# Performance work log

Measured on AMD Instinct MI355X. Metric: run time of the kernel, lower is better.

Reference implementation:

```python
import jax, jax.numpy as jnp
import numpy as np

N = 64   # SSM state size
H = 256  # channels
B = 8    # batch
L = 1024 # sequence length


def setup_inputs() -> dict:
    key = jax.random.key(0)
    k1, k2, k3, k4, k5 = jax.random.split(key, 5)
    scale = 1.0 / np.sqrt(N)  # lecun_normal std for fan_in=N
    inp = jax.random.normal(k1, (B, L, H), jnp.float32)
    As = jax.random.normal(k2, (H, N, N), jnp.float32) * scale
    Bs = jax.random.normal(k3, (H, N, 1), jnp.float32) * scale
    Cs = jax.random.normal(k4, (H, 1, N), jnp.float32) * scale
    Ds = jnp.ones((H,), jnp.float32)
    # log_step_initializer: uniform in [log(dt_min), log(dt_max)]
    lo, hi = np.log(0.001), np.log(0.003)
    log_steps = jax.random.uniform(k5, (H,), jnp.float32) * (hi - lo) + lo
    return {"inp": inp, "As": As, "Bs": Bs, "Cs": Cs, "Ds": Ds, "log_steps": log_steps}


def _discretize(A, B_, C, step):
    # Bilinear (Tustin) discretization, batched over H. step: (H,)
    I = jnp.eye(A.shape[-1], dtype=A.dtype)
    s = (step / 2.0)[:, None, None]            # (H,1,1)
    lhs = I - s * A                            # (H,N,N)
    Ab = jnp.linalg.solve(lhs, I + s * A)      # (H,N,N)
    Bb = jnp.linalg.solve(lhs, (2.0 * s) * B_) # (H,N,1)
    return Ab, Bb, C


def _kernel(Ab, Bb, Cb, length):
    # K[l] = Cb @ Ab^l @ Bb, built via a scan over matrix powers (all heads batched)
    def body(x, _):
        k = jnp.einsum('hon,hno->h', Cb, x)          # (H,)
        x_next = jnp.einsum('hmn,hno->hmo', Ab, x)   # (H,N,1)
        return x_next, k
    _, K = jax.lax.scan(body, Bb, None, length=length)
    return K  # (L, H)


def reference(inp, As, Bs, Cs, Ds, log_steps):
    Lseq = inp.shape[1]
    step = jnp.exp(log_steps)
    Ab, Bb, Cb = _discretize(As, Bs, Cs, step)
    K = _kernel(Ab, Bb, Cb, Lseq)                      # (L, H)
    # causal (non-circular) convolution via FFT, per channel
    n = 2 * Lseq
    Uf = jnp.fft.rfft(inp, n=n, axis=1)                # (B, F, H)
    Kf = jnp.fft.rfft(K, n=n, axis=0)[None]            # (1, F, H)
    y = jnp.fft.irfft(Uf * Kf, n=n, axis=1)[:, :Lseq]  # (B, L, H)
    return y + Ds[None, None, :] * inp
```

## Files before the change

kernel.cpp:

```cpp
#include <hip/hip_runtime.h>
#include <cstddef>

#define SSM_N 64
#define SSM_H 256
#define SSM_B 8
#define SSM_L 1024
#define PADM  68
#define PADC  68
#define KTP   1040

__global__ __launch_bounds__(256) void ssm_prep_kernel(
    const float* __restrict__ As, const float* __restrict__ Bsin,
    const float* __restrict__ Csin, const float* __restrict__ logsteps,
    float* __restrict__ KTout)
{
    __shared__ __align__(16) float B0[SSM_N * PADM];
    __shared__ __align__(16) float B1[SSM_N * PADM];
    __shared__ __align__(16) float CallL[32 * PADC];
    __shared__ __align__(16) float XallL[32 * PADC];
    __shared__ float pbuf[4 * 64];

    const int h    = blockIdx.x;
    const int tid  = threadIdx.x;
    const int lane = tid & 63;
    const int q    = tid >> 6;
    const int j0   = q * 16;

    const float step = expf(logsteps[h]);
    const float s    = 0.5f * step;

    float arow[64];
    {
        const float4* Ar = reinterpret_cast<const float4*>(As + (size_t)h * 4096 + lane * 64);
        #pragma unroll
        for (int r = 0; r < 16; ++r) {
            float4 v = Ar[r];
            arow[4*r+0] = s * v.x; arow[4*r+1] = s * v.y;
            arow[4*r+2] = s * v.z; arow[4*r+3] = s * v.w;
        }
        if (q == 0) {
            float4* wp = reinterpret_cast<float4*>(B1 + lane * PADM);
            #pragma unroll
            for (int r = 0; r < 16; ++r)
                wp[r] = make_float4(arow[4*r], arow[4*r+1], arow[4*r+2], arow[4*r+3]);
        }
    }
    __syncthreads();

    #pragma unroll 1
    for (int it = 0; it < 2; ++it) {
        const float* Bop = (it == 0) ? B1 : B0;
        float acc[16];
        #pragma unroll
        for (int jj = 0; jj < 16; ++jj) acc[jj] = arow[j0 + jj];
        #pragma unroll
        for (int k = 0; k < 64; ++k) {
            const float a = arow[k];
            const float4* bp = reinterpret_cast<const float4*>(Bop + k * PADM + j0);
            const float4 b0 = bp[0], b1v = bp[1], b2 = bp[2], b3 = bp[3];
            acc[0]  += a * b0.x;  acc[1]  += a * b0.y;  acc[2]  += a * b0.z;  acc[3]  += a * b0.w;
            acc[4]  += a * b1v.x; acc[5]  += a * b1v.y; acc[6]  += a * b1v.z; acc[7]  += a * b1v.w;
            acc[8]  += a * b2.x;  acc[9]  += a * b2.y;  acc[10] += a * b2.z;  acc[11] += a * b2.w;
            acc[12] += a * b3.x;  acc[13] += a * b3.y;  acc[14] += a * b3.z;  acc[15] += a * b3.w;
        }
        float4* wp = reinterpret_cast<float4*>(B0 + lane * PADM + j0);
        wp[0] = make_float4(acc[0],  acc[1],  acc[2],  acc[3]);
        wp[1] = make_float4(acc[4],  acc[5],  acc[6],  acc[7]);
        wp[2] = make_float4(acc[8],  acc[9],  acc[10], acc[11]);
        wp[3] = make_float4(acc[12], acc[13], acc[14], acc[15]);
    }
    __syncthreads();

    if (q == 0)      pbuf[lane]  = Bsin[h * SSM_N + lane];
    else if (q == 1) CallL[lane] = Csin[h * SSM_N + lane];
    #pragma unroll
    for (int r = 0; r < 16; ++r) {
        int e = r * 256 + tid, i = e >> 6, j = e & 63;
        B1[j * PADM + i] = 2.f * B0[i * PADM + j] + ((i == j) ? 1.f : 0.f);
    }
    __syncthreads();

    if (q == 0) {
        float accb = 0.f;
        #pragma unroll
        for (int r = 0; r < 16; ++r) {
            const float4 sv = *reinterpret_cast<const float4*>(B0 + lane * PADM + 4 * r);
            accb += sv.x * pbuf[4*r] + sv.y * pbuf[4*r+1] + sv.z * pbuf[4*r+2] + sv.w * pbuf[4*r+3];
        }
        XallL[lane] = step * (pbuf[lane] + accb);
    }

    #pragma unroll 1
    for (int j = 0; j < 31; ++j) {
        const float* crow = CallL + j * PADC;
        float pp = 0.f;
        #pragma unroll
        for (int r = 0; r < 4; ++r) {
            const float4 cc = *reinterpret_cast<const float4*>(crow + j0 + 4 * r);
            const float4 aa = *reinterpret_cast<const float4*>(B1 + lane * PADM + j0 + 4 * r);
            pp += cc.x * aa.x + cc.y * aa.y + cc.z * aa.z + cc.w * aa.w;
        }
        pbuf[q * 64 + lane] = pp;
        __syncthreads();
        if (q == 0)
            CallL[(j + 1) * PADC + lane] =
                pbuf[lane] + pbuf[64 + lane] + pbuf[128 + lane] + pbuf[192 + lane];
        __syncthreads();
    }

    {
        float* src = B1;
        float* dst = B0;
        #pragma unroll 1
        for (int it = 0; it < 5; ++it) {
            #pragma unroll
            for (int r = 0; r < 16; ++r) {
                const float4 v = *reinterpret_cast<const float4*>(src + lane * PADM + 4 * r);
                arow[4*r] = v.x; arow[4*r+1] = v.y; arow[4*r+2] = v.z; arow[4*r+3] = v.w;
            }
            float acc[16];
            #pragma unroll
            for (int jj = 0; jj < 16; ++jj) acc[jj] = 0.f;
            #pragma unroll
            for (int k = 0; k < 64; ++k) {
                const float a = arow[k];
                const float4* bp = reinterpret_cast<const float4*>(src + k * PADM + j0);
                const float4 b0 = bp[0], b1v = bp[1], b2 = bp[2], b3 = bp[3];
                acc[0]  += a * b0.x;  acc[1]  += a * b0.y;  acc[2]  += a * b0.z;  acc[3]  += a * b0.w;
                acc[4]  += a * b1v.x; acc[5]  += a * b1v.y; acc[6]  += a * b1v.z; acc[7]  += a * b1v.w;
                acc[8]  += a * b2.x;  acc[9]  += a * b2.y;  acc[10] += a * b2.z;  acc[11] += a * b2.w;
                acc[12] += a * b3.x;  acc[13] += a * b3.y;  acc[14] += a * b3.z;  acc[15] += a * b3.w;
            }
            float4* wp = reinterpret_cast<float4*>(dst + lane * PADM + j0);
            wp[0] = make_float4(acc[0],  acc[1],  acc[2],  acc[3]);
            wp[1] = make_float4(acc[4],  acc[5],  acc[6],  acc[7]);
            wp[2] = make_float4(acc[8],  acc[9],  acc[10], acc[11]);
            wp[3] = make_float4(acc[12], acc[13], acc[14], acc[15]);
            __syncthreads();
            float* tmp = src; src = dst; dst = tmp;
        }
    }

    #pragma unroll
    for (int r = 0; r < 16; ++r) {
        int e = r * 256 + tid, i = e >> 6, jj = e & 63;
        B1[i * PADM + jj] = B0[jj * PADM + i];
    }
    __syncthreads();

    #pragma unroll 1
    for (int m = 0; m < 31; ++m) {
        const float* xrow = XallL + m * PADC;
        float pp = 0.f;
        #pragma unroll
        for (int r = 0; r < 4; ++r) {
            const float4 xx = *reinterpret_cast<const float4*>(xrow + j0 + 4 * r);
            const float4 aa = *reinterpret_cast<const float4*>(B1 + lane * PADM + j0 + 4 * r);
            pp += xx.x * aa.x + xx.y * aa.y + xx.z * aa.z + xx.w * aa.w;
        }
        pbuf[q * 64 + lane] = pp;
        __syncthreads();
        if (q == 0)
            XallL[(m + 1) * PADC + lane] =
                pbuf[lane] + pbuf[64 + lane] + pbuf[128 + lane] + pbuf[192 + lane];
        __syncthreads();
    }

    #pragma unroll
    for (int r = 0; r < 4; ++r) {
        int l = r * 256 + tid, mm = l >> 5, jj = l & 31;
        const float4* cr = reinterpret_cast<const float4*>(CallL + jj * PADC);
        const float4* xr = reinterpret_cast<const float4*>(XallL + mm * PADC);
        float sacc = 0.f;
        #pragma unroll
        for (int i = 0; i < 16; ++i) {
            const float4 c4 = cr[i], x4 = xr[i];
            sacc += c4.x * x4.x + c4.y * x4.y + c4.z * x4.z + c4.w * x4.w;
        }
        KTout[(size_t)h * KTP + l] = sacc;
    }
}

__global__ __launch_bounds__(256) void ssm_ktr_kernel(
    const float* __restrict__ KT, float* __restrict__ K)
{
    __shared__ float tile[32][33];
    const int l0 = (blockIdx.x & 31) * 32;
    const int h0 = (blockIdx.x >> 5) * 32;
    const int c  = threadIdx.x & 31;
    const int r0 = threadIdx.x >> 5;
    #pragma unroll
    for (int k = 0; k < 4; ++k)
        tile[r0 + 8 * k][c] = KT[(size_t)(h0 + r0 + 8 * k) * KTP + l0 + c];
    __syncthreads();
    #pragma unroll
    for (int k = 0; k < 4; ++k)
        K[(size_t)(l0 + r0 + 8 * k) * SSM_H + h0 + c] = tile[c][r0 + 8 * k];
}

__global__ __launch_bounds__(256) void ssm_conv_kernel(
    const float* __restrict__ U, const float* __restrict__ Kk,
    const float* __restrict__ Ds, float* __restrict__ Y)
{
    const int h = threadIdx.x;
    const int b = blockIdx.x & 7;
    const int p = blockIdx.x >> 3;
    const float dh = Ds[h];
    const float* Ub = U + (size_t)b * SSM_L * SSM_H + h;
    float* Yb = Y + (size_t)b * SSM_L * SSM_H + h;

    #pragma unroll
    for (int half = 0; half < 2; ++half) {
        const int t  = (half == 0) ? p : (127 - p);
        const int l0 = t << 3;
        float acc[8], win[15], kreg[8], u0[8];

        #pragma unroll
        for (int j = 0; j < 15; ++j) {
            const int li = l0 - 7 + j;
            win[j] = (li >= 0) ? Ub[li * SSM_H] : 0.f;
        }
        #pragma unroll
        for (int i = 0; i < 8; ++i) { acc[i] = 0.f; u0[i] = win[7 + i]; }
        #pragma unroll
        for (int j = 0; j < 8; ++j) kreg[j] = Kk[j * SSM_H + h];

        const float* kp = Kk + 8 * SSM_H + h;
        const float* up = Ub + (l0 - 15) * SSM_H;
        #pragma unroll 2
        for (int c = 0; c < t - 1; ++c) {
            float kn[8], nw[8];
            #pragma unroll
            for (int j = 0; j < 8; ++j) kn[j] = kp[j * SSM_H];
            #pragma unroll
            for (int j = 0; j < 8; ++j) nw[j] = up[j * SSM_H];
            #pragma unroll
            for (int dd = 0; dd < 8; ++dd) {
                const float kv = kreg[dd];
                #pragma unroll
                for (int i = 0; i < 8; ++i) acc[i] += kv * win[7 + i - dd];
            }
            #pragma unroll
            for (int j = 14; j >= 8; --j) win[j] = win[j - 8];
            #pragma unroll
            for (int j = 0; j < 8; ++j) { win[j] = nw[j]; kreg[j] = kn[j]; }
            kp += 8 * SSM_H;
            up -= 8 * SSM_H;
        }

        if (t >= 1) {
            float kn[8];
            #pragma unroll
            for (int j = 0; j < 8; ++j) kn[j] = Kk[(8 * t + j) * SSM_H + h];
            const float uz = Ub[0];
            #pragma unroll
            for (int dd = 0; dd < 8; ++dd) {
                const float kv = kreg[dd];
                #pragma unroll
                for (int i = 0; i < 8; ++i) acc[i] += kv * win[7 + i - dd];
            }
            #pragma unroll
            for (int j = 14; j >= 8; --j) win[j] = win[j - 8];
            #pragma unroll
            for (int j = 0; j < 7; ++j) win[j] = 0.f;
            win[7] = uz;
            #pragma unroll
            for (int j = 0; j < 8; ++j) kreg[j] = kn[j];
        }

        #pragma unroll
        for (int dd = 0; dd < 8; ++dd) {
            const float kv = kreg[dd];
            #pragma unroll
            for (int i = 0; i < 8; ++i) acc[i] += kv * win[7 + i - dd];
        }

        #pragma unroll
        for (int i = 0; i < 8; ++i)
            Yb[(l0 + i) * SSM_H] = acc[i] + dh * u0[i];
    }
}

extern "C" void kernel_launch(void* const* d_in, const int* in_sizes, int n_in,
                              void* d_out, int out_size, void* d_ws, size_t ws_size,
                              hipStream_t stream)
{
    const float* inp    = (const float*)d_in[0];
    const float* As     = (const float*)d_in[1];
    const float* Bsin   = (const float*)d_in[2];
    const float* Csin   = (const float*)d_in[3];
    const float* Dsin   = (const float*)d_in[4];
    const float* lsteps = (const float*)d_in[5];
    float* Y    = (float*)d_out;
    float* KT   = (float*)d_out;
    float* Kbuf = (float*)d_ws;

    ssm_prep_kernel<<<dim3(SSM_H), dim3(256), 0, stream>>>(As, Bsin, Csin, lsteps, KT);
    ssm_ktr_kernel<<<dim3(256), dim3(256), 0, stream>>>(KT, Kbuf);
    ssm_conv_kernel<<<dim3(SSM_B * 64), dim3(256), 0, stream>>>(inp, Kbuf, Dsin, Y);
}
```

Baseline: 197.2 us.

## Restructure SSM prep with power-doubling Krylov and unroll conv window rotation

The prep kernel now runs with 512 threads and builds the C and X Krylov blocks by doubling (appending 2^k rows per squaring step), replacing the 31-step serial matvec loops that each needed two barriers. Squarings and block extensions are interleaved in one loop. The convolution kernel replaces the 15-element shifting window with a three-buffer rotation unrolled by three, which avoids register moves, and it rereads the input for the D term. This cuts barrier counts and serial chains in prep and register shuffling in conv, at the cost of more register pressure and some code complexity.

```diff
diff --git a/kernel.cpp b/kernel.cpp
--- a/kernel.cpp
+++ b/kernel.cpp
@@ -5,179 +5,152 @@
 #define SSM_H 256
 #define SSM_B 8
 #define SSM_L 1024
-#define PADM  68
-#define PADC  68
+#define PADB  68
 #define KTP   1040
 
-__global__ __launch_bounds__(256) void ssm_prep_kernel(
+
+__device__ __forceinline__ void load_row(const float* M, int r, float (&arow)[64])
+{
+    #pragma unroll
+    for (int q = 0; q < 16; ++q) {
+        const float4 v = *reinterpret_cast<const float4*>(M + r * PADB + 4 * q);
+        arow[4*q+0] = v.x; arow[4*q+1] = v.y; arow[4*q+2] = v.z; arow[4*q+3] = v.w;
+    }
+}
+
+__device__ __forceinline__ void mm_row8(const float (&arow)[64], const float* B,
+                                        int g8, float (&acc)[8])
+{
+    #pragma unroll
+    for (int t = 0; t < 64; ++t) {
+        const float4 b0 = *reinterpret_cast<const float4*>(B + t * PADB + g8);
+        const float4 b1 = *reinterpret_cast<const float4*>(B + t * PADB + g8 + 4);
+        const float a = arow[t];
+        acc[0] += a * b0.x; acc[1] += a * b0.y; acc[2] += a * b0.z; acc[3] += a * b0.w;
+        acc[4] += a * b1.x; acc[5] += a * b1.y; acc[6] += a * b1.z; acc[7] += a * b1.w;
+    }
+}
+
+__global__ __launch_bounds__(512) void ssm_prep_kernel(
     const float* __restrict__ As, const float* __restrict__ Bsin,
     const float* __restrict__ Csin, const float* __restrict__ logsteps,
     float* __restrict__ KTout)
 {
-    __shared__ __align__(16) float B0[SSM_N * PADM];
-    __shared__ __align__(16) float B1[SSM_N * PADM];
-    __shared__ __align__(16) float CallL[32 * PADC];
-    __shared__ __align__(16) float XallL[32 * PADC];
-    __shared__ float pbuf[4 * 64];
-
-    const int h    = blockIdx.x;
-    const int tid  = threadIdx.x;
-    const int lane = tid & 63;
-    const int q    = tid >> 6;
-    const int j0   = q * 16;
+    __shared__ __align__(16) float Ea[SSM_N * PADB];
+    __shared__ __align__(16) float Eb[SSM_N * PADB];
+    __shared__ __align__(16) float Cm[32 * PADB];
+    __shared__ __align__(16) float Xm[32 * PADB];
+    __shared__ float bvs[64];
+
+    const int h   = blockIdx.x;
+    const int tid = threadIdx.x;
+    const int r   = tid & 63;
+    const int w   = tid >> 6;
+    const int g8  = w * 8;
 
     const float step = expf(logsteps[h]);
     const float s    = 0.5f * step;
 
+    #pragma unroll
+    for (int ps = 0; ps < 2; ++ps) {
+        const float4 v = *reinterpret_cast<const float4*>(
+            As + (size_t)h * 4096 + 2048 * ps + 4 * tid);
+        const int row = 32 * ps + (tid >> 4);
+        const int col = (tid & 15) * 4;
+        *reinterpret_cast<float4*>(Ea + row * PADB + col) =
+            make_float4(s * v.x, s * v.y, s * v.z, s * v.w);
+    }
+    if (tid < 64)       Cm[tid]        = Csin[h * SSM_N + tid];
+    else if (tid < 128) bvs[tid - 64]  = Bsin[h * SSM_N + tid - 64];
+    __syncthreads();
+
     float arow[64];
-    {
-        const float4* Ar = reinterpret_cast<const float4*>(As + (size_t)h * 4096 + lane * 64);
-        #pragma unroll
-        for (int r = 0; r < 16; ++r) {
-            float4 v = Ar[r];
-            arow[4*r+0] = s * v.x; arow[4*r+1] = s * v.y;
-            arow[4*r+2] = s * v.z; arow[4*r+3] = s * v.w;
-        }
-        if (q == 0) {
-            float4* wp = reinterpret_cast<float4*>(B1 + lane * PADM);
-            #pragma unroll
-            for (int r = 0; r < 16; ++r)
-                wp[r] = make_float4(arow[4*r], arow[4*r+1], arow[4*r+2], arow[4*r+3]);
-        }
-    }
+    load_row(Ea, r, arow);
+    float acc[8];
+
+    #pragma unroll
+    for (int j = 0; j < 8; ++j) acc[j] = arow[g8 + j];
+    mm_row8(arow, Ea, g8, acc);
+    *reinterpret_cast<float4*>(Eb + r * PADB + g8)     = make_float4(acc[0], acc[1], acc[2], acc[3]);
+    *reinterpret_cast<float4*>(Eb + r * PADB + g8 + 4) = make_float4(acc[4], acc[5], acc[6], acc[7]);
     __syncthreads();
 
+    #pragma unroll
+    for (int j = 0; j < 8; ++j) acc[j] = arow[g8 + j];
+    mm_row8(arow, Eb, g8, acc);
+    #pragma unroll
+    for (int j = 0; j < 8; ++j)
+        Ea[r * PADB + g8 + j] = 2.f * acc[j] + ((r == g8 + j) ? 1.f : 0.f);
+    __syncthreads();
+
+    float* Ecur = Ea;
+    float* Enxt = Eb;
     #pragma unroll 1
-    for (int it = 0; it < 2; ++it) {
-        const float* Bop = (it == 0) ? B1 : B0;
-        float acc[16];
-        #pragma unroll
-        for (int jj = 0; jj < 16; ++jj) acc[jj] = arow[j0 + jj];
-        #pragma unroll
-        for (int k = 0; k < 64; ++k) {
-            const float a = arow[k];
-            const float4* bp = reinterpret_cast<const float4*>(Bop + k * PADM + j0);
-            const float4 b0 = bp[0], b1v = bp[1], b2 = bp[2], b3 = bp[3];
-            acc[0]  += a * b0.x;  acc[1]  += a * b0.y;  acc[2]  += a * b0.z;  acc[3]  += a * b0.w;
-            acc[4]  += a * b1v.x; acc[5]  += a * b1v.y; acc[6]  += a * b1v.z; acc[7]  += a * b1v.w;
-            acc[8]  += a * b2.x;  acc[9]  += a * b2.y;  acc[10] += a * b2.z;  acc[11] += a * b2.w;
-            acc[12] += a * b3.x;  acc[13] += a * b3.y;  acc[14] += a * b3.z;  acc[15] += a * b3.w;
-        }
-        float4* wp = reinterpret_cast<float4*>(B0 + lane * PADM + j0);
-        wp[0] = make_float4(acc[0],  acc[1],  acc[2],  acc[3]);
-        wp[1] = make_float4(acc[4],  acc[5],  acc[6],  acc[7]);
-        wp[2] = make_float4(acc[8],  acc[9],  acc[10], acc[11]);
-        wp[3] = make_float4(acc[12], acc[13], acc[14], acc[15]);
-    }
-    __syncthreads();
-
-    if (q == 0)      pbuf[lane]  = Bsin[h * SSM_N + lane];
-    else if (q == 1) CallL[lane] = Csin[h * SSM_N + lane];
-    #pragma unroll
-    for (int r = 0; r < 16; ++r) {
-        int e = r * 256 + tid, i = e >> 6, j = e & 63;
-        B1[j * PADM + i] = 2.f * B0[i * PADM + j] + ((i == j) ? 1.f : 0.f);
-    }
-    __syncthreads();
-
-    if (q == 0) {
-        float accb = 0.f;
-        #pragma unroll
-        for (int r = 0; r < 16; ++r) {
-            const float4 sv = *reinterpret_cast<const float4*>(B0 + lane * PADM + 4 * r);
-            accb += sv.x * pbuf[4*r] + sv.y * pbuf[4*r+1] + sv.z * pbuf[4*r+2] + sv.w * pbuf[4*r+3];
-        }
-        XallL[lane] = step * (pbuf[lane] + accb);
-    }
-
-    #pragma unroll 1
-    for (int j = 0; j < 31; ++j) {
-        const float* crow = CallL + j * PADC;
-        float pp = 0.f;
-        #pragma unroll
-        for (int r = 0; r < 4; ++r) {
-            const float4 cc = *reinterpret_cast<const float4*>(crow + j0 + 4 * r);
-            const float4 aa = *reinterpret_cast<const float4*>(B1 + lane * PADM + j0 + 4 * r);
-            pp += cc.x * aa.x + cc.y * aa.y + cc.z * aa.z + cc.w * aa.w;
-        }
-        pbuf[q * 64 + lane] = pp;
+    for (int k = 0; k < 10; ++k) {
+        load_row(Ecur, r, arow);
+
+        if (k == 0 && w == 0) {
+            float a = 0.f;
+            #pragma unroll
+            for (int t = 0; t < 64; ++t) a += arow[t] * bvs[t];
+            Xm[r] = s * (bvs[r] + a);
+        }
+
+        if (k <= 4) {
+            const int nj = 1 << k;
+            #pragma unroll
+            for (int rep = 0; rep < 2; ++rep) {
+                const int j = w + 8 * rep;
+                if (j < nj) {
+                    const float* crow = Cm + j * PADB;
+                    float a = 0.f;
+                    #pragma unroll
+                    for (int t = 0; t < 64; ++t)
+                        a += crow[t] * Ecur[t * PADB + r];
+                    Cm[(j + nj) * PADB + r] = a;
+                }
+            }
+        } else {
+            const int kx = k - 5;
+            const int nm = 1 << kx;
+            #pragma unroll
+            for (int rep = 0; rep < 2; ++rep) {
+                const int m = w + 8 * rep;
+                if (m < nm) {
+                    const float* xs = Xm + m * PADB;
+                    float a = 0.f;
+                    #pragma unroll
+                    for (int t = 0; t < 64; ++t)
+                        a += arow[t] * xs[t];
+                    Xm[(m + nm) * PADB + r] = a;
+                }
+            }
+        }
+
+        if (k < 9) {
+            #pragma unroll
+            for (int j = 0; j < 8; ++j) acc[j] = 0.f;
+            mm_row8(arow, Ecur, g8, acc);
+            *reinterpret_cast<float4*>(Enxt + r * PADB + g8)     = make_float4(acc[0], acc[1], acc[2], acc[3]);
+            *reinterpret_cast<float4*>(Enxt + r * PADB + g8 + 4) = make_float4(acc[4], acc[5], acc[6], acc[7]);
+        }
         __syncthreads();
-        if (q == 0)
-            CallL[(j + 1) * PADC + lane] =
-                pbuf[lane] + pbuf[64 + lane] + pbuf[128 + lane] + pbuf[192 + lane];
-        __syncthreads();
-    }
-
-    {
-        float* src = B1;
-        float* dst = B0;
-        #pragma unroll 1
-        for (int it = 0; it < 5; ++it) {
-            #pragma unroll
-            for (int r = 0; r < 16; ++r) {
-                const float4 v = *reinterpret_cast<const float4*>(src + lane * PADM + 4 * r);
-                arow[4*r] = v.x; arow[4*r+1] = v.y; arow[4*r+2] = v.z; arow[4*r+3] = v.w;
-            }
-            float acc[16];
-            #pragma unroll
-            for (int jj = 0; jj < 16; ++jj) acc[jj] = 0.f;
-            #pragma unroll
-            for (int k = 0; k < 64; ++k) {
-                const float a = arow[k];
-                const float4* bp = reinterpret_cast<const float4*>(src + k * PADM + j0);
-                const float4 b0 = bp[0], b1v = bp[1], b2 = bp[2], b3 = bp[3];
-                acc[0]  += a * b0.x;  acc[1]  += a * b0.y;  acc[2]  += a * b0.z;  acc[3]  += a * b0.w;
-                acc[4]  += a * b1v.x; acc[5]  += a * b1v.y; acc[6]  += a * b1v.z; acc[7]  += a * b1v.w;
-                acc[8]  += a * b2.x;  acc[9]  += a * b2.y;  acc[10] += a * b2.z;  acc[11] += a * b2.w;
-                acc[12] += a * b3.x;  acc[13] += a * b3.y;  acc[14] += a * b3.z;  acc[15] += a * b3.w;
-            }
-            float4* wp = reinterpret_cast<float4*>(dst + lane * PADM + j0);
-            wp[0] = make_float4(acc[0],  acc[1],  acc[2],  acc[3]);
-            wp[1] = make_float4(acc[4],  acc[5],  acc[6],  acc[7]);
-            wp[2] = make_float4(acc[8],  acc[9],  acc[10], acc[11]);
-            wp[3] = make_float4(acc[12], acc[13], acc[14], acc[15]);
-            __syncthreads();
-            float* tmp = src; src = dst; dst = tmp;
-        }
-    }
-
-    #pragma unroll
-    for (int r = 0; r < 16; ++r) {
-        int e = r * 256 + tid, i = e >> 6, jj = e & 63;
-        B1[i * PADM + jj] = B0[jj * PADM + i];
-    }
-    __syncthreads();
-
-    #pragma unroll 1
-    for (int m = 0; m < 31; ++m) {
-        const float* xrow = XallL + m * PADC;
-        float pp = 0.f;
-        #pragma unroll
-        for (int r = 0; r < 4; ++r) {
-            const float4 xx = *reinterpret_cast<const float4*>(xrow + j0 + 4 * r);
-            const float4 aa = *reinterpret_cast<const float4*>(B1 + lane * PADM + j0 + 4 * r);
-            pp += xx.x * aa.x + xx.y * aa.y + xx.z * aa.z + xx.w * aa.w;
-        }
-        pbuf[q * 64 + lane] = pp;
-        __syncthreads();
-        if (q == 0)
-            XallL[(m + 1) * PADC + lane] =
-                pbuf[lane] + pbuf[64 + lane] + pbuf[128 + lane] + pbuf[192 + lane];
-        __syncthreads();
-    }
-
-    #pragma unroll
-    for (int r = 0; r < 4; ++r) {
-        int l = r * 256 + tid, mm = l >> 5, jj = l & 31;
-        const float4* cr = reinterpret_cast<const float4*>(CallL + jj * PADC);
-        const float4* xr = reinterpret_cast<const float4*>(XallL + mm * PADC);
-        float sacc = 0.f;
+        float* tmp = Ecur; Ecur = Enxt; Enxt = tmp;
+    }
+
+    #pragma unroll
+    for (int rep = 0; rep < 2; ++rep) {
+        const int l = tid + 512 * rep;
+        const int m = l >> 5, j = l & 31;
+        const float4* cr = reinterpret_cast<const float4*>(Cm + j * PADB);
+        const float4* xr = reinterpret_cast<const float4*>(Xm + m * PADB);
+        float d = 0.f;
         #pragma unroll
         for (int i = 0; i < 16; ++i) {
             const float4 c4 = cr[i], x4 = xr[i];
-            sacc += c4.x * x4.x + c4.y * x4.y + c4.z * x4.z + c4.w * x4.w;
-        }
-        KTout[(size_t)h * KTP + l] = sacc;
+            d += c4.x * x4.x + c4.y * x4.y + c4.z * x4.z + c4.w * x4.w;
+        }
+        KTout[(size_t)h * KTP + l] = d;
     }
 }
 
@@ -196,6 +169,28 @@
     #pragma unroll
     for (int k = 0; k < 4; ++k)
         K[(size_t)(l0 + r0 + 8 * k) * SSM_H + h0 + c] = tile[c][r0 + 8 * k];
+}
+
+
+__device__ __forceinline__ void ld8(float (&d)[8], const float* base)
+{
+    #pragma unroll
+    for (int j = 0; j < 8; ++j) d[j] = base[j * SSM_H];
+}
+
+__device__ __forceinline__ void fma8(float (&acc)[8], const float (&kv)[8],
+                                     const float (&cur)[8], const float (&prv)[8])
+{
+    #pragma unroll
+    for (int dd = 0; dd < 8; ++dd) {
+        const float k = kv[dd];
+        #pragma unroll
+        for (int i = 0; i < 8; ++i) {
+            const int idx = 7 + i - dd;
+            const float u = (idx < 8) ? cur[idx] : prv[idx - 8];
+            acc[i] += k * u;
+        }
+    }
 }
 
 __global__ __launch_bounds__(256) void ssm_conv_kernel(
@@ -211,39 +206,56 @@
 
     #pragma unroll
     for (int half = 0; half < 2; ++half) {
-        const int t  = (half == 0) ? p : (127 - p);
+        const int t  = half ? (127 - p) : p;
         const int l0 = t << 3;
-        float acc[8], win[15], kreg[8], u0[8];
-
-        #pragma unroll
-        for (int j = 0; j < 15; ++j) {
-            const int li = l0 - 7 + j;
-            win[j] = (li >= 0) ? Ub[li * SSM_H] : 0.f;
-        }
-        #pragma unroll
-        for (int i = 0; i < 8; ++i) { acc[i] = 0.f; u0[i] = win[7 + i]; }
-        #pragma unroll
-        for (int j = 0; j < 8; ++j) kreg[j] = Kk[j * SSM_H + h];
-
+
+        float acc[8];
+        #pragma unroll
+        for (int i = 0; i < 8; ++i) acc[i] = 0.f;
+
+        float kA[8], wA[8], wB[8];
+        if (t == 0) {
+            #pragma unroll
+            for (int j = 0; j < 8; ++j) wA[j] = 0.f;
+            wA[7] = Ub[0];
+        } else {
+            #pragma unroll
+            for (int j = 0; j < 8; ++j) wA[j] = Ub[(l0 - 7 + j) * SSM_H];
+        }
+        #pragma unroll
+        for (int j = 0; j < 7; ++j) wB[j] = Ub[(l0 + 1 + j) * SSM_H];
+        wB[7] = 0.f;
+        ld8(kA, Kk + h);
+
+        const int nclean = (t >= 1) ? (t - 1) : 0;
+        const int n3 = nclean - (nclean % 3);
         const float* kp = Kk + 8 * SSM_H + h;
-        const float* up = Ub + (l0 - 15) * SSM_H;
-        #pragma unroll 2
-        for (int c = 0; c < t - 1; ++c) {
+        const float* up = Ub + (ptrdiff_t)(l0 - 15) * SSM_H;
+
+        int c = 0;
+        #pragma unroll 1
+        for (; c < n3; c += 3) {
+            float kB[8], kC[8], wC[8];
+            ld8(kB, kp);
+            ld8(wC, up);
+            fma8(acc, kA, wA, wB);
+            ld8(kC, kp + 8 * SSM_H);
+            ld8(wB, up - 8 * SSM_H);
+            fma8(acc, kB, wC, wA);
+            ld8(kA, kp + 16 * SSM_H);
+            ld8(wA, up - 16 * SSM_H);
+            fma8(acc, kC, wB, wC);
+            kp += 24 * SSM_H;
+            up -= 24 * SSM_H;
+        }
+        #pragma unroll 1
+        for (; c < nclean; ++c) {
             float kn[8], nw[8];
-            #pragma unroll
-            for (int j = 0; j < 8; ++j) kn[j] = kp[j * SSM_H];
-            #pragma unroll
-            for (int j = 0; j < 8; ++j) nw[j] = up[j * SSM_H];
-            #pragma unroll
-            for (int dd = 0; dd < 8; ++dd) {
-                const float kv = kreg[dd];
-                #pragma unroll
-                for (int i = 0; i < 8; ++i) acc[i] += kv * win[7 + i - dd];
-            }
-            #pragma unroll
-            for (int j = 14; j >= 8; --j) win[j] = win[j - 8];
-            #pragma unroll
-            for (int j = 0; j < 8; ++j) { win[j] = nw[j]; kreg[j] = kn[j]; }
+            ld8(kn, kp);
+            ld8(nw, up);
+            fma8(acc, kA, wA, wB);
+            #pragma unroll
+            for (int j = 0; j < 8; ++j) { wB[j] = wA[j]; wA[j] = nw[j]; kA[j] = kn[j]; }
             kp += 8 * SSM_H;
             up -= 8 * SSM_H;
         }
@@ -253,31 +265,24 @@
             #pragma unroll
             for (int j = 0; j < 8; ++j) kn[j] = Kk[(8 * t + j) * SSM_H + h];
             const float uz = Ub[0];
+            fma8(acc, kA, wA, wB);
             #pragma unroll
             for (int dd = 0; dd < 8; ++dd) {
-                const float kv = kreg[dd];
+                const float k = kn[dd];
                 #pragma unroll
-                for (int i = 0; i < 8; ++i) acc[i] += kv * win[7 + i - dd];
+                for (int i = 0; i < 8; ++i) {
+                    const int idx = 7 + i - dd;
+                    if (idx == 7)      acc[i] += k * uz;
+                    else if (idx > 7)  acc[i] += k * wA[idx - 8];
+                }
             }
-            #pragma unroll
-            for (int j = 14; j >= 8; --j) win[j] = win[j - 8];
-            #pragma unroll
-            for (int j = 0; j < 7; ++j) win[j] = 0.f;
-            win[7] = uz;
-            #pragma unroll
-            for (int j = 0; j < 8; ++j) kreg[j] = kn[j];
-        }
-
-        #pragma unroll
-        for (int dd = 0; dd < 8; ++dd) {
-            const float kv = kreg[dd];
-            #pragma unroll
-            for (int i = 0; i < 8; ++i) acc[i] += kv * win[7 + i - dd];
+        } else {
+            fma8(acc, kA, wA, wB);
         }
 
         #pragma unroll
         for (int i = 0; i < 8; ++i)
-            Yb[(l0 + i) * SSM_H] = acc[i] + dh * u0[i];
+            Yb[(l0 + i) * SSM_H] = acc[i] + dh * Ub[(l0 + i) * SSM_H];
     }
 }
 
@@ -295,7 +300,7 @@
     float* KT   = (float*)d_out;
     float* Kbuf = (float*)d_ws;
 
-    ssm_prep_kernel<<<dim3(SSM_H), dim3(256), 0, stream>>>(As, Bsin, Csin, lsteps, KT);
+    ssm_prep_kernel<<<dim3(SSM_H), dim3(512), 0, stream>>>(As, Bsin, Csin, lsteps, KT);
     ssm_ktr_kernel<<<dim3(256), dim3(256), 0, stream>>>(KT, Kbuf);
-    ssm_conv_kernel<<<dim3(SSM_B * 64), dim3(256), 0, stream>>>(inp, Kbuf, Dsin, Y);
-}
+    ssm_conv_kernel<<<dim3(512), dim3(256), 0, stream>>>(inp, Kbuf, Dsin, Y);
+}
```

Result: slower. 203.3 us (+3.1%).
